# Performance work log

Measured on AMD Instinct MI355X. Metric: run time of the kernel, lower is better.

## Reference

```python
import jax, jax.numpy as jnp
import numpy as np
from jax import lax

B, C, H, W, K = 16, 64, 192, 192, 11
EPS = 1e-5


def _depthwise(x, w, pad):
    # x: (B,C,h,w), w: (C,1,kh,kw), pad: ((ph,ph),(pw,pw))
    return lax.conv_general_dilated(
        x, w, window_strides=(1, 1), padding=pad,
        feature_group_count=x.shape[1],
        dimension_numbers=('NCHW', 'OIHW', 'NCHW'))


def _maxpool3(x):
    return lax.reduce_window(x, -jnp.inf, lax.max,
                             (1, 1, 3, 3), (1, 1, 1, 1),
                             ((0, 0), (0, 0), (1, 1), (1, 1)))


def _blurpool(x):
    # filt_size=4, stride=3, reflect pad (1,2) on each spatial dim
    a = jnp.array([1., 3., 3., 1.], dtype=x.dtype)
    f = a[:, None] * a[None, :]
    f = f / f.sum()
    filt = jnp.tile(f[None, None], (x.shape[1], 1, 1, 1))  # (C,1,4,4)
    xp = jnp.pad(x, ((0, 0), (0, 0), (1, 2), (1, 2)), mode='reflect')
    return lax.conv_general_dilated(
        xp, filt, window_strides=(3, 3), padding='VALID',
        feature_group_count=x.shape[1],
        dimension_numbers=('NCHW', 'OIHW', 'NCHW'))


def _h_transform(x):
    b, c, h, w = x.shape
    x = jnp.pad(x, ((0, 0), (0, 0), (0, 0), (0, w)))
    x = x.reshape(b, c, -1)[..., :-w]
    return x.reshape(b, c, h, 2 * w - 1)


def _inv_h_transform(x):
    b, c, h, l = x.shape
    x = x.reshape(b, c, -1)
    x = jnp.pad(x, ((0, 0), (0, 0), (0, h)))
    x = x.reshape(b, c, h, 2 * h)
    return x[..., :h]


def _v_transform(x):
    return _h_transform(x.transpose(0, 1, 3, 2)).transpose(0, 1, 3, 2)


def _inv_v_transform(x):
    return _inv_h_transform(x.transpose(0, 1, 3, 2)).transpose(0, 1, 3, 2)


def _mra(x, w_h1, w_v1, w_h2, w_v2, bn_gamma, bn_beta, bn_mean, bn_var):
    kp = K // 2
    x_tem = _blurpool(_maxpool3(x))                 # (B,C,h,h), h=64
    x_h1 = _depthwise(x_tem, w_h1, ((kp, kp), (1, 1)))
    x_w1 = _depthwise(x_tem, w_v1, ((1, 1), (kp, kp)))
    x_h2 = _inv_h_transform(_depthwise(_h_transform(x_tem), w_h2, ((kp, kp), (1, 1))))
    x_w2 = _inv_v_transform(_depthwise(_v_transform(x_tem), w_v2, ((1, 1), (kp, kp))))
    att = x_h1 + x_w1 + x_h2 + x_w2
    # inference-mode BatchNorm2d
    inv = bn_gamma / jnp.sqrt(bn_var + EPS)
    att = att * inv[None, :, None, None] + (bn_beta - bn_mean * inv)[None, :, None, None]
    gate = jax.nn.sigmoid(att)                      # (B,C,h,h)
    # nearest-neighbor upsample to (H,W): torch idx = floor(i*h/H)
    h = gate.shape[-2]
    ih = (jnp.arange(H) * h) // H
    iw = (jnp.arange(W) * gate.shape[-1]) // W
    gate_up = gate[:, :, ih][:, :, :, iw]           # (B,C,H,W)
    return x[:, :C] * gate_up


def setup_inputs() -> dict:
    key = jax.random.key(0)
    ks = jax.random.split(key, 9)
    x = jax.random.normal(ks[0], (B, C, H, W), jnp.float32)
    w_h1 = jax.random.normal(ks[1], (C, 1, K, 3), jnp.float32) * 0.05
    w_v1 = jax.random.normal(ks[2], (C, 1, 3, K), jnp.float32) * 0.05
    w_h2 = jax.random.normal(ks[3], (C, 1, K, 3), jnp.float32) * 0.05
    w_v2 = jax.random.normal(ks[4], (C, 1, 3, K), jnp.float32) * 0.05
    bn_gamma = jnp.ones((C,), jnp.float32)
    bn_beta = jnp.zeros((C,), jnp.float32)
    bn_mean = jax.random.normal(ks[5], (C,), jnp.float32) * 0.1
    bn_var = jax.random.uniform(ks[6], (C,), jnp.float32, 0.5, 1.5)
    return {'x': x, 'w_h1': w_h1, 'w_v1': w_v1, 'w_h2': w_h2, 'w_v2': w_v2,
            'bn_gamma': bn_gamma, 'bn_beta': bn_beta,
            'bn_mean': bn_mean, 'bn_var': bn_var}


def reference(x, w_h1, w_v1, w_h2, w_v2, bn_gamma, bn_beta, bn_mean, bn_var):
    return _mra(x, w_h1, w_v1, w_h2, w_v2, bn_gamma, bn_beta, bn_mean, bn_var)
```

## Files before the change

### kernel.cpp

```cpp
#include <hip/hip_runtime.h>
#include <math.h>

__global__ __launch_bounds__(256) void k1_pool(const float* __restrict__ x,
                                               float* __restrict__ xtem) {
    const int plane = blockIdx.y;
    const int i0 = blockIdx.x * 4;
    const int base = 3 * i0 - 2;

    __shared__ float xs[15 * 192];

    const float* xp = x + (size_t)plane * (192 * 192);
    for (int f = threadIdx.x; f < 15 * 48; f += 256) {
        int r = f / 48, c4 = f - r * 48;
        int src = min(max(base + r, 0), 191);
        ((float4*)xs)[f] = ((const float4*)(xp + (size_t)src * 192))[c4];
    }
    __syncthreads();

    const int j = threadIdx.x & 63;
    const int il = threadIdx.x >> 6;
    const int i = i0 + il;

    int colk[6];
#pragma unroll
    for (int k = 0; k < 6; ++k)
        colk[k] = min(max(3 * j - 2 + k, 0), 191);

    float vmu[4][6];
#pragma unroll
    for (int k = 0; k < 6; ++k) {
        const float* cp = xs + 3 * il * 192 + colk[k];
        float p0 = cp[0 * 192], p1 = cp[1 * 192], p2 = cp[2 * 192];
        float p3 = cp[3 * 192], p4 = cp[4 * 192], p5 = cp[5 * 192];
        float q1 = fmaxf(p1, p2), q2 = fmaxf(p2, p3);
        float q3 = fmaxf(p3, p4), q4 = fmaxf(p4, p5);
        vmu[0][k] = fmaxf(p0, q1);
        vmu[1][k] = fmaxf(p1, q2);
        vmu[2][k] = fmaxf(p2, q3);
        vmu[3][k] = fmaxf(p3, q4);
    }

    float cbv[4];
#pragma unroll
    for (int u = 0; u < 4; ++u) {
        float g1 = fmaxf(vmu[u][1], vmu[u][2]);
        float g2 = fmaxf(vmu[u][2], vmu[u][3]);
        float g3 = fmaxf(vmu[u][3], vmu[u][4]);
        float g4 = fmaxf(vmu[u][4], vmu[u][5]);
        float h0 = fmaxf(vmu[u][0], g1);
        float h1 = fmaxf(vmu[u][1], g2);
        float h2 = fmaxf(vmu[u][2], g3);
        float h3 = fmaxf(vmu[u][3], g4);
        float ha = (j == 0) ? h2 : h0;
        cbv[u] = ha + 3.f * h1 + 3.f * h2 + h3;
    }
    float c0 = (i == 0) ? cbv[2] : cbv[0];
    float acc = c0 + 3.f * cbv[1] + 3.f * cbv[2] + cbv[3];
    xtem[(size_t)plane * 4096 + i * 64 + j] = acc * (1.f / 64.f);
}

__global__ __launch_bounds__(256) void k2_att(
    const float* __restrict__ xtem,
    const float* __restrict__ wh1g, const float* __restrict__ wv1g,
    const float* __restrict__ wh2g, const float* __restrict__ wv2g,
    const float* __restrict__ gamma, const float* __restrict__ beta,
    const float* __restrict__ mean, const float* __restrict__ var,
    float* __restrict__ gate) {
    const int plane = blockIdx.x;
    const int c = plane & 63;
    __shared__ float T[64 * 80];
    __shared__ float att[64 * 64];

    for (int e = threadIdx.x; e < 64 * 80; e += 256) T[e] = 0.f;
    __syncthreads();
    for (int e = threadIdx.x; e < 4096; e += 256)
        T[(e >> 6) * 80 + 6 + (e & 63)] = xtem[(size_t)plane * 4096 + e];

    const float inv = gamma[c] * rsqrtf(var[c] + 1e-5f);
    const float bias = beta[c] - mean[c] * inv;
    __syncthreads();

    const int j = threadIdx.x & 63;
    const int ib = (threadIdx.x >> 6) * 16;

    float Wa[33], Wb[33];
    float acc[13];

#pragma unroll
    for (int k = 0; k < 33; ++k) {
        Wa[k] = wh1g[c * 33 + k];
        Wb[k] = wh2g[c * 33 + k];
    }
#pragma unroll
    for (int k = 0; k < 13; ++k) acc[k] = 0.f;
    for (int t = ib - 6; t <= ib + 21; ++t) {
        if (t >= 0 && t < 64) {
            float w_[13];
#pragma unroll
            for (int d = 0; d < 13; ++d) w_[d] = T[t * 80 + j + d];
#pragma unroll
            for (int p = 0; p < 11; ++p) {
                acc[11 - p] += Wa[p * 3 + 0] * w_[5] + Wa[p * 3 + 1] * w_[6] +
                               Wa[p * 3 + 2] * w_[7] +
                               Wb[p * 3 + 0] * w_[10 - p] +
                               Wb[p * 3 + 1] * w_[11 - p] +
                               Wb[p * 3 + 2] * w_[12 - p];
            }
        }
        int i = t - 6;
        if (i >= ib) att[i * 64 + j] = acc[0];
#pragma unroll
        for (int k = 0; k < 12; ++k) acc[k] = acc[k + 1];
        acc[12] = 0.f;
    }

#pragma unroll
    for (int k = 0; k < 33; ++k) {
        Wa[k] = wv1g[c * 33 + k];
        Wb[k] = wv2g[c * 33 + k];
    }
#pragma unroll
    for (int k = 0; k < 13; ++k) acc[k] = 0.f;
    float* gp = gate + (size_t)plane * 4096;
    for (int t = ib - 6; t <= ib + 21; ++t) {
        if (t >= 0 && t < 64) {
            float w_[13];
#pragma unroll
            for (int d = 0; d < 13; ++d) w_[d] = T[t * 80 + j + d];
#pragma unroll
            for (int p = 0; p < 3; ++p) {
#pragma unroll
                for (int q = 0; q < 11; ++q) {
                    acc[7 - p] += Wa[p * 11 + q] * w_[q + 1];
                    acc[2 - p + q] += Wb[p * 11 + q] * w_[q + 1];
                }
            }
        }
        int i = t - 6;
        if (i >= ib) {
            float z = (att[i * 64 + j] + acc[0]) * inv + bias;
            gp[i * 64 + j] = 1.f / (1.f + __expf(-z));
        }
#pragma unroll
        for (int k = 0; k < 12; ++k) acc[k] = acc[k + 1];
        acc[12] = 0.f;
    }
}

__global__ __launch_bounds__(256) void k3_mul(const float* __restrict__ x,
                                              const float* __restrict__ gate,
                                              float* __restrict__ out) {
    int idx = blockIdx.x * 256 + threadIdx.x;
    int j4 = idx % 48;
    int rest = idx / 48;
    int i = rest % 192;
    int plane = rest / 192;
    float4 xv = ((const float4*)x)[idx];
    const float* gp = gate + (size_t)plane * 4096 + (i / 3) * 64;
    int jj = 4 * j4;
    int g0 = jj / 3;
    int r = jj - 3 * g0;
    float ga = gp[g0], gb = gp[g0 + 1];
    float4 o;
    o.x = xv.x * ga;
    o.y = xv.y * (r == 2 ? gb : ga);
    o.z = xv.z * (r == 0 ? ga : gb);
    o.w = xv.w * gb;
    ((float4*)out)[idx] = o;
}

extern "C" void kernel_launch(void* const* d_in, const int* in_sizes, int n_in,
                              void* d_out, int out_size, void* d_ws, size_t ws_size,
                              hipStream_t stream) {
    const float* x     = (const float*)d_in[0];
    const float* wh1   = (const float*)d_in[1];
    const float* wv1   = (const float*)d_in[2];
    const float* wh2   = (const float*)d_in[3];
    const float* wv2   = (const float*)d_in[4];
    const float* gamma = (const float*)d_in[5];
    const float* beta  = (const float*)d_in[6];
    const float* mean  = (const float*)d_in[7];
    const float* var   = (const float*)d_in[8];
    float* out  = (float*)d_out;
    float* xtem = (float*)d_ws;
    float* gate = xtem + (size_t)1024 * 4096;

    k1_pool<<<dim3(16, 1024), 256, 0, stream>>>(x, xtem);
    k2_att<<<1024, 256, 0, stream>>>(xtem, wh1, wv1, wh2, wv2,
                                     gamma, beta, mean, var, gate);
    k3_mul<<<36864, 256, 0, stream>>>(x, gate, out);
}
```

Before: 334.7 us.

## Fuse gate computation with upsample-multiply and use rotating accumulator registers

Merges the attention/gate kernel with the final upsample-and-multiply kernel, so each block keeps its gate plane in shared memory and streams the corresponding x plane to the output, removing the gate round-trip through global memory and one launch. Also fully unrolls the row loops and indexes the accumulator ring by modulo at compile time instead of shifting registers each step. The risks are that the multiply phase now runs on only 1024 blocks with a long serial per-block tail, and the larger unrolled code raises register pressure.

```diff
diff --git a/kernel.cpp b/kernel.cpp
--- a/kernel.cpp
+++ b/kernel.cpp
@@ -59,13 +59,13 @@
     xtem[(size_t)plane * 4096 + i * 64 + j] = acc * (1.f / 64.f);
 }
 
-__global__ __launch_bounds__(256) void k2_att(
-    const float* __restrict__ xtem,
+__global__ __launch_bounds__(256) void k2_att_mul(
+    const float* __restrict__ xtem, const float* __restrict__ x,
     const float* __restrict__ wh1g, const float* __restrict__ wv1g,
     const float* __restrict__ wh2g, const float* __restrict__ wv2g,
     const float* __restrict__ gamma, const float* __restrict__ beta,
     const float* __restrict__ mean, const float* __restrict__ var,
-    float* __restrict__ gate) {
+    float* __restrict__ out) {
     const int plane = blockIdx.x;
     const int c = plane & 63;
     __shared__ float T[64 * 80];
@@ -82,9 +82,10 @@
 
     const int j = threadIdx.x & 63;
     const int ib = (threadIdx.x >> 6) * 16;
+    const int t0 = ib - 6;
 
     float Wa[33], Wb[33];
-    float acc[13];
+    float racc[13];
 
 #pragma unroll
     for (int k = 0; k < 33; ++k) {
@@ -92,26 +93,29 @@
         Wb[k] = wh2g[c * 33 + k];
     }
 #pragma unroll
-    for (int k = 0; k < 13; ++k) acc[k] = 0.f;
-    for (int t = ib - 6; t <= ib + 21; ++t) {
+    for (int k = 0; k < 13; ++k) racc[k] = 0.f;
+#pragma unroll
+    for (int tt = 0; tt < 28; ++tt) {
+        const int t = t0 + tt;
         if (t >= 0 && t < 64) {
             float w_[13];
 #pragma unroll
             for (int d = 0; d < 13; ++d) w_[d] = T[t * 80 + j + d];
 #pragma unroll
             for (int p = 0; p < 11; ++p) {
-                acc[11 - p] += Wa[p * 3 + 0] * w_[5] + Wa[p * 3 + 1] * w_[6] +
-                               Wa[p * 3 + 2] * w_[7] +
-                               Wb[p * 3 + 0] * w_[10 - p] +
-                               Wb[p * 3 + 1] * w_[11 - p] +
-                               Wb[p * 3 + 2] * w_[12 - p];
+                racc[(tt + 11 - p) % 13] +=
+                    Wa[p * 3 + 0] * w_[5] + Wa[p * 3 + 1] * w_[6] +
+                    Wa[p * 3 + 2] * w_[7] +
+                    Wb[p * 3 + 0] * w_[10 - p] +
+                    Wb[p * 3 + 1] * w_[11 - p] +
+                    Wb[p * 3 + 2] * w_[12 - p];
             }
         }
-        int i = t - 6;
-        if (i >= ib) att[i * 64 + j] = acc[0];
-#pragma unroll
-        for (int k = 0; k < 12; ++k) acc[k] = acc[k + 1];
-        acc[12] = 0.f;
+        if (tt >= 12) {
+            const int i = t - 6;
+            att[i * 64 + j] = racc[tt % 13];
+        }
+        racc[tt % 13] = 0.f;
     }
 
 #pragma unroll
@@ -120,9 +124,10 @@
         Wb[k] = wv2g[c * 33 + k];
     }
 #pragma unroll
-    for (int k = 0; k < 13; ++k) acc[k] = 0.f;
-    float* gp = gate + (size_t)plane * 4096;
-    for (int t = ib - 6; t <= ib + 21; ++t) {
+    for (int k = 0; k < 13; ++k) racc[k] = 0.f;
+#pragma unroll
+    for (int tt = 0; tt < 28; ++tt) {
+        const int t = t0 + tt;
         if (t >= 0 && t < 64) {
             float w_[13];
 #pragma unroll
@@ -131,42 +136,47 @@
             for (int p = 0; p < 3; ++p) {
 #pragma unroll
                 for (int q = 0; q < 11; ++q) {
-                    acc[7 - p] += Wa[p * 11 + q] * w_[q + 1];
-                    acc[2 - p + q] += Wb[p * 11 + q] * w_[q + 1];
+                    racc[(tt + 7 - p) % 13] += Wa[p * 11 + q] * w_[q + 1];
+                    racc[(tt + 2 - p + q) % 13] += Wb[p * 11 + q] * w_[q + 1];
                 }
             }
         }
-        int i = t - 6;
-        if (i >= ib) {
-            float z = (att[i * 64 + j] + acc[0]) * inv + bias;
-            gp[i * 64 + j] = 1.f / (1.f + __expf(-z));
-        }
-#pragma unroll
-        for (int k = 0; k < 12; ++k) acc[k] = acc[k + 1];
-        acc[12] = 0.f;
-    }
-}
-
-__global__ __launch_bounds__(256) void k3_mul(const float* __restrict__ x,
-                                              const float* __restrict__ gate,
-                                              float* __restrict__ out) {
-    int idx = blockIdx.x * 256 + threadIdx.x;
-    int j4 = idx % 48;
-    int rest = idx / 48;
-    int i = rest % 192;
-    int plane = rest / 192;
-    float4 xv = ((const float4*)x)[idx];
-    const float* gp = gate + (size_t)plane * 4096 + (i / 3) * 64;
-    int jj = 4 * j4;
-    int g0 = jj / 3;
-    int r = jj - 3 * g0;
-    float ga = gp[g0], gb = gp[g0 + 1];
-    float4 o;
-    o.x = xv.x * ga;
-    o.y = xv.y * (r == 2 ? gb : ga);
-    o.z = xv.z * (r == 0 ? ga : gb);
-    o.w = xv.w * gb;
-    ((float4*)out)[idx] = o;
+        if (tt >= 12) {
+            const int i = t - 6;
+            float z = (att[i * 64 + j] + racc[tt % 13]) * inv + bias;
+            att[i * 64 + j] = 1.f / (1.f + __expf(-z));
+        }
+        racc[tt % 13] = 0.f;
+    }
+    __syncthreads();
+
+    const float4* xp4 = (const float4*)(x + (size_t)plane * 36864);
+    float4* op4 = (float4*)(out + (size_t)plane * 36864);
+#pragma unroll
+    for (int bse = 0; bse < 9216; bse += 1024) {
+        float4 xv[4];
+        int e[4];
+#pragma unroll
+        for (int u = 0; u < 4; ++u) {
+            e[u] = bse + u * 256 + threadIdx.x;
+            xv[u] = xp4[e[u]];
+        }
+#pragma unroll
+        for (int u = 0; u < 4; ++u) {
+            int i = e[u] / 48, c4 = e[u] - i * 48;
+            const float* gp = att + (i / 3) * 64;
+            int jj = 4 * c4;
+            int g0 = jj / 3;
+            int r = jj - 3 * g0;
+            float ga = gp[g0], gb = gp[g0 + 1];
+            float4 o;
+            o.x = xv[u].x * ga;
+            o.y = xv[u].y * (r == 2 ? gb : ga);
+            o.z = xv[u].z * (r == 0 ? ga : gb);
+            o.w = xv[u].w * gb;
+            op4[e[u]] = o;
+        }
+    }
 }
 
 extern "C" void kernel_launch(void* const* d_in, const int* in_sizes, int n_in,
@@ -183,10 +193,8 @@
     const float* var   = (const float*)d_in[8];
     float* out  = (float*)d_out;
     float* xtem = (float*)d_ws;
-    float* gate = xtem + (size_t)1024 * 4096;
 
     k1_pool<<<dim3(16, 1024), 256, 0, stream>>>(x, xtem);
-    k2_att<<<1024, 256, 0, stream>>>(xtem, wh1, wv1, wh2, wv2,
-                                     gamma, beta, mean, var, gate);
-    k3_mul<<<36864, 256, 0, stream>>>(x, gate, out);
+    k2_att_mul<<<1024, 256, 0, stream>>>(xtem, x, wh1, wv1, wh2, wv2,
+                                         gamma, beta, mean, var, out);
 }
```

After: 320.8 us. -4.1%, faster.
